# Kernel tuning notes

Measured on AMD Instinct MI355X. Metric: run time of the kernel, lower is better.

The kernel has to match this reference:

```python
import jax, jax.numpy as jnp
import numpy as np

REP_THR = 0.6
BORDER = 10


def setup_inputs() -> dict:
    key = jax.random.key(0)
    repeatability = jax.random.uniform(key, (8, 1, 2048, 2048), dtype=jnp.float32)
    return {"repeatability": repeatability}


def reference(repeatability):
    # 3x3 max pool, stride 1, pad 1 (torch pads with -inf for max pool)
    local_max = jax.lax.reduce_window(
        repeatability,
        -jnp.inf,
        jax.lax.max,
        window_dimensions=(1, 1, 3, 3),
        window_strides=(1, 1, 1, 1),
        padding=[(0, 0), (0, 0), (1, 1), (1, 1)],
    )
    maxima = (repeatability == local_max) & (repeatability >= REP_THR)
    # border mask: zero out a 10-pixel frame
    B, C, H, W = repeatability.shape
    border = jnp.zeros((H, W), dtype=bool).at[BORDER:-BORDER, BORDER:-BORDER].set(True)
    maxima = maxima & border  # broadcast over (B, C)
    # Original returns maxima.nonzero().t()[2:4] (data-dependent shape);
    # for jit-compatibility we return the dense boolean mask as float32 —
    # the (y, x) indices are exactly the nonzero positions of this mask.
    return maxima.astype(jnp.float32)
```

## Files before the change

kernel.cpp:

```cpp
#include <hip/hip_runtime.h>
#include <math.h>

#define IMG_H 2048
#define IMG_W 2048
#define NB    8
#define BORDER 10
#define REP_THR 0.6f

__global__ __launch_bounds__(256) void nms_kernel(const float* __restrict__ in,
                                                  float* __restrict__ out) {
    const int tid = blockIdx.x * blockDim.x + threadIdx.x;
    const int gx = tid & 255;
    const int gy = (tid >> 8) & 511;
    const int b  = tid >> 17;

    const int x8 = gx << 3;
    const int y0 = gy << 2;

    const size_t img_off = (size_t)b * IMG_H * IMG_W;
    float* obase = out + img_off + (size_t)y0 * IMG_W + x8;

    if (gx == 0 || gx == 255 || gy <= 1 || gy >= 510) {
        const float4 z = make_float4(0.f, 0.f, 0.f, 0.f);
#pragma unroll
        for (int j = 0; j < 4; ++j) {
            *(float4*)(obase + (size_t)j * IMG_W)     = z;
            *(float4*)(obase + (size_t)j * IMG_W + 4) = z;
        }
        return;
    }

    const float* ibase = in + img_off + (size_t)(y0 - 1) * IMG_W + x8;

    float h[6][8];
    float c[4][8];
#pragma unroll
    for (int r = 0; r < 6; ++r) {
        const float* row = ibase + (size_t)r * IMG_W;
        const float4 L = *(const float4*)(row - 4);
        const float4 M = *(const float4*)(row);
        const float4 N = *(const float4*)(row + 4);
        const float4 R = *(const float4*)(row + 8);

        h[r][0] = fmaxf(L.w, fmaxf(M.x, M.y));
        h[r][1] = fmaxf(M.x, fmaxf(M.y, M.z));
        h[r][2] = fmaxf(M.y, fmaxf(M.z, M.w));
        h[r][3] = fmaxf(M.z, fmaxf(M.w, N.x));
        h[r][4] = fmaxf(M.w, fmaxf(N.x, N.y));
        h[r][5] = fmaxf(N.x, fmaxf(N.y, N.z));
        h[r][6] = fmaxf(N.y, fmaxf(N.z, N.w));
        h[r][7] = fmaxf(N.z, fmaxf(N.w, R.x));

        if (r >= 1 && r <= 4) {
            c[r - 1][0] = M.x; c[r - 1][1] = M.y; c[r - 1][2] = M.z; c[r - 1][3] = M.w;
            c[r - 1][4] = N.x; c[r - 1][5] = N.y; c[r - 1][6] = N.z; c[r - 1][7] = N.w;
        }
    }

    bool bx[8];
#pragma unroll
    for (int p = 0; p < 8; ++p)
        bx[p] = (x8 + p >= BORDER) && (x8 + p < IMG_W - BORDER);

#pragma unroll
    for (int j = 0; j < 4; ++j) {
        const int y = y0 + j;
        const bool rowok = (y >= BORDER) && (y < IMG_H - BORDER);

        float r0[8];
#pragma unroll
        for (int p = 0; p < 8; ++p) {
            const float m = fmaxf(h[j][p], fmaxf(h[j + 1][p], h[j + 2][p]));
            r0[p] = (c[j][p] == m && c[j][p] >= REP_THR && bx[p] && rowok) ? 1.f : 0.f;
        }
        float4 lo = make_float4(r0[0], r0[1], r0[2], r0[3]);
        float4 hi = make_float4(r0[4], r0[5], r0[6], r0[7]);
        *(float4*)(obase + (size_t)j * IMG_W)     = lo;
        *(float4*)(obase + (size_t)j * IMG_W + 4) = hi;
    }
}

extern "C" void kernel_launch(void* const* d_in, const int* in_sizes, int n_in,
                              void* d_out, int out_size, void* d_ws, size_t ws_size,
                              hipStream_t stream) {
    const float* in = (const float*)d_in[0];
    float* out = (float*)d_out;
    const int total_threads = NB * (IMG_H / 4) * (IMG_W / 8);
    const int block = 256;
    const int grid = total_threads / block;
    nms_kernel<<<grid, block, 0, stream>>>(in, out);
}
```

Measured before the change: 234.1 us.

## Stage full-width row bands in LDS via direct global-to-LDS loads

Each block now handles an 8-row, full-width band of one image. It copies the 10 input rows (band plus halo) into LDS using global_load_lds and then computes the 3x3 max from LDS. This cuts redundant global reads of halo rows, since the halo overhead drops from 6/4 to 10/8 rows, and removes horizontal halo reloads. In exchange it uses 80KB of LDS per block, which limits occupancy, and adds a block-wide barrier with no overlap between loading and compute.

```diff
diff --git a/kernel.cpp b/kernel.cpp
--- a/kernel.cpp
+++ b/kernel.cpp
@@ -1,42 +1,69 @@
 #include <hip/hip_runtime.h>
 #include <math.h>
+#include <stdint.h>
 
 #define IMG_H 2048
 #define IMG_W 2048
 #define NB    8
 #define BORDER 10
 #define REP_THR 0.6f
+#define BAND   8
+#define SROWS  (BAND + 2)
+#define NBANDS (IMG_H / BAND)
 
-__global__ __launch_bounds__(256) void nms_kernel(const float* __restrict__ in,
-                                                  float* __restrict__ out) {
-    const int tid = blockIdx.x * blockDim.x + threadIdx.x;
-    const int gx = tid & 255;
-    const int gy = (tid >> 8) & 511;
-    const int b  = tid >> 17;
 
-    const int x8 = gx << 3;
-    const int y0 = gy << 2;
+typedef __attribute__((address_space(3))) uint32_t       lds_u32_t;
+typedef const __attribute__((address_space(1))) uint32_t glob_u32_t;
 
+__global__ __launch_bounds__(256, 2) void nms_kernel(const float* __restrict__ in,
+                                                     float* __restrict__ out) {
+    extern __shared__ float lds[];
+
+    const int s = blockIdx.x & (NBANDS - 1);
+    const int b = blockIdx.x >> 8;
+    const int y0 = s * BAND;
     const size_t img_off = (size_t)b * IMG_H * IMG_W;
-    float* obase = out + img_off + (size_t)y0 * IMG_W + x8;
+    const int t = threadIdx.x;
 
-    if (gx == 0 || gx == 255 || gy <= 1 || gy >= 510) {
+    float* oband = out + img_off + (size_t)y0 * IMG_W;
+
+    if (s == 0 || s == NBANDS - 1) {
         const float4 z = make_float4(0.f, 0.f, 0.f, 0.f);
 #pragma unroll
-        for (int j = 0; j < 4; ++j) {
-            *(float4*)(obase + (size_t)j * IMG_W)     = z;
-            *(float4*)(obase + (size_t)j * IMG_W + 4) = z;
+        for (int k = 0; k < 16; ++k)
+            *(float4*)(oband + (size_t)(k * 256 + t) * 4) = z;
+        return;
+    }
+
+    const float* region = in + img_off + (size_t)(y0 - 1) * IMG_W;
+    const int wave = t >> 6;
+    const int lane = t & 63;
+#pragma unroll
+    for (int i = 0; i < SROWS * IMG_W / 256 / 4; ++i) {
+        const int c = i * 4 + wave;
+        glob_u32_t* g = (glob_u32_t*)(region + c * 256 + lane * 4);
+        lds_u32_t*  l = (lds_u32_t*)(lds + c * 256 + lane * 4);
+        __builtin_amdgcn_global_load_lds(g, l, 16, 0, 0);
+    }
+    __syncthreads();
+
+    const int x8 = t << 3;
+
+    if (t == 0 || t == 255) {
+        const float4 z = make_float4(0.f, 0.f, 0.f, 0.f);
+#pragma unroll
+        for (int j = 0; j < BAND; ++j) {
+            *(float4*)(oband + (size_t)j * IMG_W + x8)     = z;
+            *(float4*)(oband + (size_t)j * IMG_W + x8 + 4) = z;
         }
         return;
     }
 
-    const float* ibase = in + img_off + (size_t)(y0 - 1) * IMG_W + x8;
-
-    float h[6][8];
-    float c[4][8];
+    float h[SROWS][8];
+    float cv[BAND][8];
 #pragma unroll
-    for (int r = 0; r < 6; ++r) {
-        const float* row = ibase + (size_t)r * IMG_W;
+    for (int r = 0; r < SROWS; ++r) {
+        const float* row = lds + r * IMG_W + x8;
         const float4 L = *(const float4*)(row - 4);
         const float4 M = *(const float4*)(row);
         const float4 N = *(const float4*)(row + 4);
@@ -51,9 +78,9 @@
         h[r][6] = fmaxf(N.y, fmaxf(N.z, N.w));
         h[r][7] = fmaxf(N.z, fmaxf(N.w, R.x));
 
-        if (r >= 1 && r <= 4) {
-            c[r - 1][0] = M.x; c[r - 1][1] = M.y; c[r - 1][2] = M.z; c[r - 1][3] = M.w;
-            c[r - 1][4] = N.x; c[r - 1][5] = N.y; c[r - 1][6] = N.z; c[r - 1][7] = N.w;
+        if (r >= 1 && r <= BAND) {
+            cv[r-1][0] = M.x; cv[r-1][1] = M.y; cv[r-1][2] = M.z; cv[r-1][3] = M.w;
+            cv[r-1][4] = N.x; cv[r-1][5] = N.y; cv[r-1][6] = N.z; cv[r-1][7] = N.w;
         }
     }
 
@@ -63,7 +90,7 @@
         bx[p] = (x8 + p >= BORDER) && (x8 + p < IMG_W - BORDER);
 
 #pragma unroll
-    for (int j = 0; j < 4; ++j) {
+    for (int j = 0; j < BAND; ++j) {
         const int y = y0 + j;
         const bool rowok = (y >= BORDER) && (y < IMG_H - BORDER);
 
@@ -71,12 +98,10 @@
 #pragma unroll
         for (int p = 0; p < 8; ++p) {
             const float m = fmaxf(h[j][p], fmaxf(h[j + 1][p], h[j + 2][p]));
-            r0[p] = (c[j][p] == m && c[j][p] >= REP_THR && bx[p] && rowok) ? 1.f : 0.f;
+            r0[p] = (cv[j][p] == m && cv[j][p] >= REP_THR && bx[p] && rowok) ? 1.f : 0.f;
         }
-        float4 lo = make_float4(r0[0], r0[1], r0[2], r0[3]);
-        float4 hi = make_float4(r0[4], r0[5], r0[6], r0[7]);
-        *(float4*)(obase + (size_t)j * IMG_W)     = lo;
-        *(float4*)(obase + (size_t)j * IMG_W + 4) = hi;
+        *(float4*)(oband + (size_t)j * IMG_W + x8)     = make_float4(r0[0], r0[1], r0[2], r0[3]);
+        *(float4*)(oband + (size_t)j * IMG_W + x8 + 4) = make_float4(r0[4], r0[5], r0[6], r0[7]);
     }
 }
 
@@ -85,8 +110,7 @@
                               hipStream_t stream) {
     const float* in = (const float*)d_in[0];
     float* out = (float*)d_out;
-    const int total_threads = NB * (IMG_H / 4) * (IMG_W / 8);
-    const int block = 256;
-    const int grid = total_threads / block;
-    nms_kernel<<<grid, block, 0, stream>>>(in, out);
+    const int grid = NB * NBANDS;
+    const size_t shmem = (size_t)SROWS * IMG_W * 4;
+    nms_kernel<<<grid, 256, shmem, stream>>>(in, out);
 }
```

Result: no change. 232.9 us (-0.5%).
